# Optimization experiments

Measured on AMD Instinct MI355X. Metric: run time of the kernel, lower is better.

## Reference

```python
import jax, jax.numpy as jnp
import numpy as np

Q, M, KLEN, B = 512, 512, 1024, 4
D, H, DH, G = 1024, 16, 64, 4
DG = D // G          # 256
EPS = 1e-6
SCALE = 1.0 / DH ** 0.5


def _group_ln(x, gamma, beta, n_group):
    # x: [L, B, D]; torch std is unbiased (ddof=1); note (x-mean)/(std+eps)
    L, b, d = x.shape
    xg = x.reshape(L, b, n_group, d // n_group)
    mean = xg.mean(-1, keepdims=True)
    std = jnp.std(xg, axis=-1, ddof=1, keepdims=True)
    out = ((xg - mean) / (std + EPS)).reshape(L, b, d)
    return gamma * out + beta


def _rel_shift(x):
    # x: [q, r, b, n]
    q, r = x.shape[0], x.shape[1]
    zero_pad = jnp.zeros((q, 1) + x.shape[2:], x.dtype)
    x_padded = jnp.concatenate([zero_pad, x], axis=1).reshape((r + 1, q) + x.shape[2:])
    return x_padded[1:].reshape(x.shape)


def setup_inputs() -> dict:
    key = jax.random.key(0)
    ks = jax.random.split(key, 14)
    p = lambda k, s: jax.random.normal(k, s, jnp.float32) * 0.02
    w = jax.random.normal(ks[0], (Q, B, D), jnp.float32)
    r = jax.random.normal(ks[1], (KLEN, 1, D), jnp.float32)
    mems = jax.random.normal(ks[2], (M, B, D), jnp.float32)
    r_w_bias = p(ks[3], (H, DH))
    r_r_bias = p(ks[4], (H, DH))
    gamma_q = jnp.ones((D,), jnp.float32); beta_q = jnp.zeros((D,), jnp.float32)
    gamma_kv = jnp.ones((D,), jnp.float32); beta_kv = jnp.zeros((D,), jnp.float32)
    Wq = p(ks[5], (G, DG, DG))       # grouped conv1d k=1: per-group [out,in]
    Wiq = p(ks[6], (DG, D))          # inter_q_net: conv1d groups=1 [out,in]
    Wk = p(ks[7], (D, D))
    Wv = p(ks[8], (D, D))
    Wr = p(ks[9], (G, DG, DG))       # r_net grouped (n_head*d_head == d_model)
    Wintra = p(ks[10], (G, DG, DG))  # intra_linear grouped conv
    Winter = p(ks[11], (DG, D))      # inter_linear nn.Linear weight
    i = jnp.arange(Q)[:, None]
    j = jnp.arange(KLEN)[None, :]
    attn_mask = (j > i + M)[:, :, None]  # [Q, KLEN, 1] bool, True = masked
    return dict(w=w, r=r, r_w_bias=r_w_bias, r_r_bias=r_r_bias, mems=mems,
                gamma_q=gamma_q, beta_q=beta_q, gamma_kv=gamma_kv, beta_kv=beta_kv,
                Wq=Wq, Wiq=Wiq, Wk=Wk, Wv=Wv, Wr=Wr, Wintra=Wintra, Winter=Winter,
                attn_mask=attn_mask)


def reference(w, r, r_w_bias, r_r_bias, mems, gamma_q, beta_q, gamma_kv, beta_kv,
              Wq, Wiq, Wk, Wv, Wr, Wintra, Winter, attn_mask):
    qlen, bsz, _ = w.shape
    rlen = r.shape[0]
    w_norm = _group_ln(w, gamma_q, beta_q, G)                       # [Q,B,D]
    kv = jnp.concatenate([mems, w], axis=0)
    kv_norm = gamma_kv * (kv - kv.mean(-1, keepdims=True)) / (
        jnp.std(kv, axis=-1, ddof=1, keepdims=True) + EPS) + beta_kv  # [K,B,D]

    # grouped 1x1 conv projections == per-group matmuls
    q_intra = jnp.einsum('qbgd,god->qbgo', w_norm.reshape(qlen, bsz, G, DG), Wq)
    q_global = jnp.einsum('qbd,od->qbo', w_norm, Wiq)               # [Q,B,DG]
    head_q = (q_intra + q_global[:, :, None, :]).reshape(qlen, bsz, H, DH)
    klen = kv_norm.shape[0]
    head_k = jnp.einsum('kbd,od->kbo', kv_norm, Wk).reshape(klen, bsz, H, DH)
    head_v = jnp.einsum('kbd,od->kbo', kv_norm, Wv).reshape(klen, bsz, H, DH)
    r_head_k = jnp.einsum('rgd,god->rgo', r[:, 0].reshape(rlen, G, DG), Wr)
    r_head_k = r_head_k.reshape(rlen, H, DH)                        # [R,H,DH]

    AC = jnp.einsum('ibnd,jbnd->ijbn', head_q + r_w_bias, head_k)
    BD = _rel_shift(jnp.einsum('ibnd,jnd->ijbn', head_q + r_r_bias, r_head_k))
    attn_score = (AC + BD) * SCALE                                  # [Q,K,B,H]
    attn_score = jnp.where(attn_mask[:, :, :, None], -jnp.inf, attn_score)
    attn_prob = jax.nn.softmax(attn_score, axis=1)
    attn_vec = jnp.einsum('ijbn,jbnd->ibnd', attn_prob, head_v)
    attn_out = attn_vec.reshape(qlen, bsz, D)

    inter = jnp.einsum('qbd,od->qbo', attn_out, Winter)             # [Q,B,DG]
    intra = jnp.einsum('qbgd,god->qbgo', attn_out.reshape(qlen, bsz, G, DG), Wintra)
    out = (intra + inter[:, :, None, :]).reshape(qlen, bsz, D)
    return w + out
```

## Files before the change

kernel.cpp:

```cpp
#include <hip/hip_runtime.h>
#include <math.h>

#define Q_LEN 512
#define M_LEN 512
#define KL    1024
#define BSZ   4
#define DM    1024
#define NH    16
#define DHD   64
#define NG    4
#define DGRP  256
#define RL    1024
#define LN_EPS 1e-6f
#define ATT_SCALE 0.125f

typedef short s16x8 __attribute__((ext_vector_type(8)));
typedef float f32x4 __attribute__((ext_vector_type(4)));

__device__ __forceinline__ float wave_sum64(float v) {
#pragma unroll
    for (int off = 32; off > 0; off >>= 1) v += __shfl_xor(v, off);
    return v;
}

__device__ __forceinline__ ushort f2bf(float f) {
    unsigned u = __float_as_uint(f);
    unsigned r = (u + 0x7fffu + ((u >> 16) & 1u)) >> 16;
    return (ushort)r;
}
__device__ __forceinline__ float bf2f(ushort u) {
    return __uint_as_float(((unsigned)u) << 16);
}

__global__ __launch_bounds__(256) void cast8_kernel(
    const float* p0, const float* p1, const float* p2, const float* p3,
    const float* p4, const float* p5, const float* p6, const float* p7,
    ushort* d0, ushort* d1, ushort* d2, ushort* d3,
    ushort* d4, ushort* d5, ushort* d6, ushort* d7)
{
    int bid = blockIdx.x;
    const float* s; ushort* d; int off;
    if      (bid < 1024) { s = p0; d = d0; off = bid; }
    else if (bid < 2048) { s = p1; d = d1; off = bid - 1024; }
    else if (bid < 3072) { s = p2; d = d2; off = bid - 2048; }
    else if (bid < 3328) { s = p3; d = d3; off = bid - 3072; }
    else if (bid < 3584) { s = p4; d = d4; off = bid - 3328; }
    else if (bid < 3840) { s = p5; d = d5; off = bid - 3584; }
    else if (bid < 4096) { s = p6; d = d6; off = bid - 3840; }
    else                 { s = p7; d = d7; off = bid - 4096; }
    int i = off * 1024 + threadIdx.x * 4;
    float4 v = *(const float4*)(s + i);
    ushort4 o;
    o.x = f2bf(v.x); o.y = f2bf(v.y); o.z = f2bf(v.z); o.w = f2bf(v.w);
    *(ushort4*)(d + i) = o;
}

__global__ __launch_bounds__(64) void group_ln_kernel(
    const float* __restrict__ w, const float* __restrict__ gamma,
    const float* __restrict__ beta, ushort* __restrict__ out)
{
    int bid = blockIdx.x;
    int g = bid & (NG - 1);
    long long row = bid >> 2;
    int t = threadIdx.x;
    long long base = row * DM + g * DGRP + t * 4;
    float4 x = *(const float4*)(w + base);
    float mean = wave_sum64(x.x + x.y + x.z + x.w) * (1.0f / 256.0f);
    float dx = x.x - mean, dy = x.y - mean, dz = x.z - mean, dw = x.w - mean;
    float ss = wave_sum64(dx * dx + dy * dy + dz * dz + dw * dw);
    float inv = 1.0f / (sqrtf(ss * (1.0f / 255.0f)) + LN_EPS);
    int db = g * DGRP + t * 4;
    float4 ga = *(const float4*)(gamma + db);
    float4 be = *(const float4*)(beta + db);
    ushort4 o;
    o.x = f2bf(ga.x * (dx * inv) + be.x);
    o.y = f2bf(ga.y * (dy * inv) + be.y);
    o.z = f2bf(ga.z * (dz * inv) + be.z);
    o.w = f2bf(ga.w * (dw * inv) + be.w);
    *(ushort4*)(out + base) = o;
}

__global__ __launch_bounds__(256) void kv_ln_kernel(
    const float* __restrict__ mems, const float* __restrict__ w,
    const float* __restrict__ gamma, const float* __restrict__ beta,
    ushort* __restrict__ out)
{
    int row = blockIdx.x;
    int k = row >> 2, b = row & 3;
    const float* src = (k < M_LEN) ? (mems + ((long long)k * BSZ + b) * DM)
                                   : (w + ((long long)(k - M_LEN) * BSZ + b) * DM);
    int t = threadIdx.x;
    float4 x = *(const float4*)(src + t * 4);
    __shared__ float red[4];
    float s = wave_sum64(x.x + x.y + x.z + x.w);
    int wv = t >> 6, ln = t & 63;
    if (ln == 0) red[wv] = s;
    __syncthreads();
    float mean = (red[0] + red[1] + red[2] + red[3]) * (1.0f / 1024.0f);
    float dx = x.x - mean, dy = x.y - mean, dz = x.z - mean, dw = x.w - mean;
    float ss = wave_sum64(dx * dx + dy * dy + dz * dz + dw * dw);
    __syncthreads();
    if (ln == 0) red[wv] = ss;
    __syncthreads();
    float var = (red[0] + red[1] + red[2] + red[3]) * (1.0f / 1023.0f);
    float inv = 1.0f / (sqrtf(var) + LN_EPS);
    int db = t * 4;
    float4 ga = *(const float4*)(gamma + db);
    float4 be = *(const float4*)(beta + db);
    ushort4 o;
    o.x = f2bf(ga.x * (dx * inv) + be.x);
    o.y = f2bf(ga.y * (dy * inv) + be.y);
    o.z = f2bf(ga.z * (dz * inv) + be.z);
    o.w = f2bf(ga.w * (dw * inv) + be.w);
    *(ushort4*)(out + (long long)row * DM + db) = o;
}

__global__ __launch_bounds__(256) void gemm_bf16_nt(
    const ushort* __restrict__ A, long long aZ, int lda,
    const ushort* __restrict__ W, long long wZ, int ldw,
    float* __restrict__ C, ushort* __restrict__ Cb, long long cZ, int ldc,
    int M, int N, int K,
    const float* __restrict__ add1, long long a1Z, int lda1,
    const float* __restrict__ add2, long long a2Z, int lda2)
{
    int z = blockIdx.z;
    A += (long long)z * aZ;
    W += (long long)z * wZ;
    if (C)  C += (long long)z * cZ;
    if (Cb) Cb += (long long)z * cZ;
    if (add1) add1 += (long long)z * a1Z;
    if (add2) add2 += (long long)z * a2Z;
    int m0 = blockIdx.y * 64, n0 = blockIdx.x * 64;
    int t = threadIdx.x;
    int lane = t & 63, wid = t >> 6;
    int wr = wid >> 1, wc = wid & 1;
    int srow = t >> 2, scol = (t & 3) * 16;
    int fr = lane & 15, kq = (lane >> 4) * 8;

    __shared__ __align__(16) ushort As[64][72];
    __shared__ __align__(16) ushort Ws[64][72];

    f32x4 acc00 = {}, acc01 = {}, acc10 = {}, acc11 = {};

    const ushort* Arow = A + (long long)(m0 + srow) * lda + scol;
    const ushort* Wrow = W + (long long)(n0 + srow) * ldw + scol;

    s16x8 ra0 = *(const s16x8*)Arow;
    s16x8 ra1 = *(const s16x8*)(Arow + 8);
    s16x8 rw0 = *(const s16x8*)Wrow;
    s16x8 rw1 = *(const s16x8*)(Wrow + 8);
    *(s16x8*)&As[srow][scol] = ra0; *(s16x8*)&As[srow][scol + 8] = ra1;
    *(s16x8*)&Ws[srow][scol] = rw0; *(s16x8*)&Ws[srow][scol + 8] = rw1;
    __syncthreads();

    for (int k0 = 0; k0 < K; k0 += 64) {
        bool hasNext = (k0 + 64) < K;
        if (hasNext) {
            ra0 = *(const s16x8*)(Arow + k0 + 64);
            ra1 = *(const s16x8*)(Arow + k0 + 72);
            rw0 = *(const s16x8*)(Wrow + k0 + 64);
            rw1 = *(const s16x8*)(Wrow + k0 + 72);
        }
#pragma unroll
        for (int kk = 0; kk < 64; kk += 32) {
            s16x8 a0 = *(const s16x8*)&As[wr * 32 + fr][kk + kq];
            s16x8 a1 = *(const s16x8*)&As[wr * 32 + 16 + fr][kk + kq];
            s16x8 b0 = *(const s16x8*)&Ws[wc * 32 + fr][kk + kq];
            s16x8 b1 = *(const s16x8*)&Ws[wc * 32 + 16 + fr][kk + kq];
            acc00 = __builtin_amdgcn_mfma_f32_16x16x32_bf16(a0, b0, acc00, 0, 0, 0);
            acc01 = __builtin_amdgcn_mfma_f32_16x16x32_bf16(a0, b1, acc01, 0, 0, 0);
            acc10 = __builtin_amdgcn_mfma_f32_16x16x32_bf16(a1, b0, acc10, 0, 0, 0);
            acc11 = __builtin_amdgcn_mfma_f32_16x16x32_bf16(a1, b1, acc11, 0, 0, 0);
        }
        __syncthreads();
        if (hasNext) {
            *(s16x8*)&As[srow][scol] = ra0; *(s16x8*)&As[srow][scol + 8] = ra1;
            *(s16x8*)&Ws[srow][scol] = rw0; *(s16x8*)&Ws[srow][scol + 8] = rw1;
            __syncthreads();
        }
    }

    int rbase = (lane >> 4) * 4;
#pragma unroll
    for (int p = 0; p < 4; ++p) {
        int mrow0 = wr * 32 + rbase + p;
        int mrow1 = mrow0 + 16;
        int ncol0 = wc * 32 + fr;
        int ncol1 = ncol0 + 16;
        float v00 = acc00[p], v01 = acc01[p], v10 = acc10[p], v11 = acc11[p];
        long long r0 = m0 + mrow0, r1 = m0 + mrow1;
        int c0 = n0 + ncol0, c1 = n0 + ncol1;
        if (add1) {
            v00 += add1[r0 * lda1 + c0]; v01 += add1[r0 * lda1 + c1];
            v10 += add1[r1 * lda1 + c0]; v11 += add1[r1 * lda1 + c1];
        }
        if (add2) {
            v00 += add2[r0 * lda2 + c0]; v01 += add2[r0 * lda2 + c1];
            v10 += add2[r1 * lda2 + c0]; v11 += add2[r1 * lda2 + c1];
        }
        if (Cb) {
            Cb[r0 * ldc + c0] = f2bf(v00); Cb[r0 * ldc + c1] = f2bf(v01);
            Cb[r1 * ldc + c0] = f2bf(v10); Cb[r1 * ldc + c1] = f2bf(v11);
        } else {
            C[r0 * ldc + c0] = v00; C[r0 * ldc + c1] = v01;
            C[r1 * ldc + c0] = v10; C[r1 * ldc + c1] = v11;
        }
    }
}

__global__ __launch_bounds__(256) void transpose_v_kernel(
    const ushort* __restrict__ vin, ushort* __restrict__ vout)
{
    __shared__ __align__(16) ushort T[64][72];
    int bn = blockIdx.y;
    int b = bn >> 4, n = bn & 15;
    int k0 = blockIdx.x * 64;
    int t = threadIdx.x;
    {
        int kr = t >> 2, dp = (t & 3) * 16;
        const ushort* sp = vin + (((long long)(k0 + kr)) * 4 + b) * DM + n * DHD + dp;
        *(s16x8*)&T[kr][dp] = *(const s16x8*)sp;
        *(s16x8*)&T[kr][dp + 8] = *(const s16x8*)(sp + 8);
    }
    __syncthreads();
    {
        int d = t >> 2, kp = (t & 3) * 16;
        ushort vals[16];
#pragma unroll
        for (int q = 0; q < 16; ++q) vals[q] = T[kp + q][d];
        ushort* dp = vout + ((long long)bn * DHD + d) * KL + k0 + kp;
        *(s16x8*)dp = *(const s16x8*)&vals[0];
        *(s16x8*)(dp + 8) = *(const s16x8*)&vals[8];
    }
}

__global__ __launch_bounds__(256) void corr_kernel(
    const ushort* __restrict__ r_hk, const float* __restrict__ rwb,
    const float* __restrict__ rrb, float* __restrict__ corr)
{
    int n = blockIdx.y;
    int k = blockIdx.x * 4 + (threadIdx.x >> 6);
    int d = threadIdx.x & 63;
    float diff = rrb[n * DHD + d] - rwb[n * DHD + d];
    float v = diff * bf2f(r_hk[(long long)k * DM + n * DHD + d]);
    v = wave_sum64(v);
    if (d == 0) corr[n * RL + k] = v;
}

__global__ __launch_bounds__(256) void attn_mfma_kernel(
    const ushort* __restrict__ hq, const ushort* __restrict__ hk,
    const ushort* __restrict__ hvT, const ushort* __restrict__ rhk,
    const float* __restrict__ corr, ushort* __restrict__ attn_out)
{
    __shared__ __align__(16) ushort Ks[2][64][72];
    __shared__ __align__(16) ushort VsT[2][64][72];
    __shared__ __align__(16) ushort RKs[128][72];
    __shared__ __align__(16) ushort BDs[64][128];
    __shared__ __align__(16) ushort Ps[64][64];

    int bh = blockIdx.y;
    int b = bh >> 4, n = bh & 15;
    int i0 = blockIdx.x * 64;
    int t = threadIdx.x;
    int lane = t & 63, w = t >> 6;
    int lr16 = lane & 15;
    int lk8 = (lane >> 4) * 8;
    int orow = (lane >> 4) * 4;
    int swzBD = ((lane >> 4) & 3) << 4;

    s16x8 qf0, qf1;
    {
        const ushort* qp = hq + (((long long)(i0 + w * 16 + lr16)) * 4 + b) * DM
                              + n * DHD + lk8;
        qf0 = *(const s16x8*)qp;
        qf1 = *(const s16x8*)(qp + 32);
    }

    f32x4 O[4] = {};
    float m_[4], l_[4];
#pragma unroll
    for (int r = 0; r < 4; ++r) { m_[r] = -INFINITY; l_[r] = 0.0f; }

    int nJ = ((i0 + 575) >> 6) + 1;
    if (nJ > 16) nJ = 16;
    int ka0 = 448 - i0;

    int srow = t >> 2, sdp = (t & 3) * 16;

    {
        const ushort* kp = hk + (((long long)srow) * 4 + b) * DM + n * DHD + sdp;
        *(s16x8*)&Ks[0][srow][sdp] = *(const s16x8*)kp;
        *(s16x8*)&Ks[0][srow][sdp + 8] = *(const s16x8*)(kp + 8);
        const ushort* vp = hvT + ((long long)bh * DHD + srow) * KL + sdp;
        *(s16x8*)&VsT[0][srow][sdp] = *(const s16x8*)vp;
        *(s16x8*)&VsT[0][srow][sdp + 8] = *(const s16x8*)(vp + 8);
        int rr = t >> 1, dp2 = (t & 1) * 32;
        int rabs = ka0 + rr;
        const ushort* rp = rhk + (long long)rabs * DM + n * DHD + dp2;
        int phys = rabs & 127;
#pragma unroll
        for (int q = 0; q < 4; ++q)
            *(s16x8*)&RKs[phys][dp2 + q * 8] = *(const s16x8*)(rp + q * 8);
    }
    __syncthreads();

    int cur = 0;
    for (int jt = 0; jt < nJ; ++jt) {
        int j0 = jt * 64;
        int ka = ka0 + j0;
        bool hasNext = (jt + 1) < nJ;

        s16x8 pk0 = {}, pk1 = {}, pv0 = {}, pv1 = {}, pr0 = {}, pr1 = {};
        if (hasNext) {
            int j0n = j0 + 64;
            const ushort* kp = hk + (((long long)(j0n + srow)) * 4 + b) * DM + n * DHD + sdp;
            pk0 = *(const s16x8*)kp;
            pk1 = *(const s16x8*)(kp + 8);
            const ushort* vp = hvT + ((long long)bh * DHD + srow) * KL + j0n + sdp;
            pv0 = *(const s16x8*)vp;
            pv1 = *(const s16x8*)(vp + 8);
            int rnew = ka + 128 + srow;
            if (rnew < RL) {
                const ushort* rp = rhk + (long long)rnew * DM + n * DHD + sdp;
                pr0 = *(const s16x8*)rp;
                pr1 = *(const s16x8*)(rp + 8);
            }
        }

        f32x4 ac[4] = {};
#pragma unroll
        for (int nb = 0; nb < 4; ++nb) {
            s16x8 kb0 = *(const s16x8*)&Ks[cur][nb * 16 + lr16][lk8];
            s16x8 kb1 = *(const s16x8*)&Ks[cur][nb * 16 + lr16][32 + lk8];
            ac[nb] = __builtin_amdgcn_mfma_f32_16x16x32_bf16(qf0, kb0, ac[nb], 0, 0, 0);
            ac[nb] = __builtin_amdgcn_mfma_f32_16x16x32_bf16(qf1, kb1, ac[nb], 0, 0, 0);
        }
        int nb0 = (jt == 0) ? 0 : 4;
        for (int nb = nb0; nb < 8; ++nb) {
            int kk = nb * 16 + lr16;
            int rabs = ka + kk;
            int phys = rabs & 127;
            f32x4 bd = {};
            s16x8 rb0 = *(const s16x8*)&RKs[phys][lk8];
            s16x8 rb1 = *(const s16x8*)&RKs[phys][32 + lk8];
            bd = __builtin_amdgcn_mfma_f32_16x16x32_bf16(qf0, rb0, bd, 0, 0, 0);
            bd = __builtin_amdgcn_mfma_f32_16x16x32_bf16(qf1, rb1, bd, 0, 0, 0);
            float cadd = (rabs < RL) ? corr[n * RL + rabs] : 0.0f;
            int colw = phys ^ swzBD;
#pragma unroll
            for (int reg = 0; reg < 4; ++reg)
                BDs[w * 16 + orow + reg][colw] = f2bf(bd[reg] + cadd);
        }
        if (jt == 0) __syncthreads();

        float pvv[4][4], rowm[4];
#pragma unroll
        for (int reg = 0; reg < 4; ++reg) {
            int il = w * 16 + orow + reg;
            int i = i0 + il;
            rowm[reg] = -INFINITY;
#pragma unroll
            for (int nb = 0; nb < 4; ++nb) {
                int jc = nb * 16 + lr16;
                int j = j0 + jc;
                float s = -INFINITY;
                if (j <= i + M_LEN) {
                    int phys = (j + 511 - i) & 127;
                    s = (ac[nb][reg] + bf2f(BDs[il][phys ^ swzBD])) * ATT_SCALE;
                }
                pvv[reg][nb] = s;
                rowm[reg] = fmaxf(rowm[reg], s);
            }
        }
#pragma unroll
        for (int st = 1; st <= 8; st <<= 1)
#pragma unroll
            for (int reg = 0; reg < 4; ++reg)
                rowm[reg] = fmaxf(rowm[reg], __shfl_xor(rowm[reg], st));
        float rs[4], alpha[4];
#pragma unroll
        for (int reg = 0; reg < 4; ++reg) {
            int il = w * 16 + orow + reg;
            float newm = fmaxf(m_[reg], rowm[reg]);
            alpha[reg] = __expf(m_[reg] - newm);
            m_[reg] = newm;
            rs[reg] = 0.0f;
#pragma unroll
            for (int nb = 0; nb < 4; ++nb) {
                float p = __expf(pvv[reg][nb] - newm);
                rs[reg] += p;
                int jc = nb * 16 + lr16;
                int colp = (((jc >> 3) ^ (il & 7)) << 3) | (jc & 7);
                Ps[il][colp] = f2bf(p);
            }
        }
#pragma unroll
        for (int st = 1; st <= 8; st <<= 1)
#pragma unroll
            for (int reg = 0; reg < 4; ++reg)
                rs[reg] += __shfl_xor(rs[reg], st);
#pragma unroll
        for (int reg = 0; reg < 4; ++reg) {
            l_[reg] = l_[reg] * alpha[reg] + rs[reg];
#pragma unroll
            for (int nb = 0; nb < 4; ++nb) O[nb][reg] *= alpha[reg];
        }

        {
            int prow = w * 16 + lr16;
            int rh = prow & 7;
#pragma unroll
            for (int kc = 0; kc < 2; ++kc) {
                int blk = kc * 4 + (lane >> 4);
                s16x8 pa = *(const s16x8*)&Ps[prow][(blk ^ rh) << 3];
#pragma unroll
                for (int nb = 0; nb < 4; ++nb) {
                    s16x8 vb = *(const s16x8*)&VsT[cur][nb * 16 + lr16][kc * 32 + lk8];
                    O[nb] = __builtin_amdgcn_mfma_f32_16x16x32_bf16(pa, vb, O[nb], 0, 0, 0);
                }
            }
        }

        if (hasNext) {
            *(s16x8*)&Ks[cur ^ 1][srow][sdp] = pk0;
            *(s16x8*)&Ks[cur ^ 1][srow][sdp + 8] = pk1;
            *(s16x8*)&VsT[cur ^ 1][srow][sdp] = pv0;
            *(s16x8*)&VsT[cur ^ 1][srow][sdp + 8] = pv1;
            int phys = (ka + 128 + srow) & 127;
            *(s16x8*)&RKs[phys][sdp] = pr0;
            *(s16x8*)&RKs[phys][sdp + 8] = pr1;
        }
        __syncthreads();
        cur ^= 1;
    }

#pragma unroll
    for (int reg = 0; reg < 4; ++reg) {
        int il = w * 16 + orow + reg;
        long long i = i0 + il;
        float inv = 1.0f / l_[reg];
#pragma unroll
        for (int nb = 0; nb < 4; ++nb)
            attn_out[(i * 4 + b) * DM + n * DHD + nb * 16 + lr16] = f2bf(O[nb][reg] * inv);
    }
}

extern "C" void kernel_launch(void* const* d_in, const int* in_sizes, int n_in,
                              void* d_out, int out_size, void* d_ws, size_t ws_size,
                              hipStream_t stream) {
    const float* w       = (const float*)d_in[0];
    const float* r       = (const float*)d_in[1];
    const float* rwb     = (const float*)d_in[2];
    const float* rrb     = (const float*)d_in[3];
    const float* mems    = (const float*)d_in[4];
    const float* gamma_q = (const float*)d_in[5];
    const float* beta_q  = (const float*)d_in[6];
    const float* gamma_kv= (const float*)d_in[7];
    const float* beta_kv = (const float*)d_in[8];
    const float* Wq      = (const float*)d_in[9];
    const float* Wiq     = (const float*)d_in[10];
    const float* Wk      = (const float*)d_in[11];
    const float* Wv      = (const float*)d_in[12];
    const float* Wr      = (const float*)d_in[13];
    const float* Wintra  = (const float*)d_in[14];
    const float* Winter  = (const float*)d_in[15];
    float* out = (float*)d_out;
    float* ws = (float*)d_ws;

    float* tmp  = ws;
    float* corr = tmp + 524288;

    ushort* w_norm_bf  = (ushort*)(corr + 16384);
    ushort* kv_norm_bf = w_norm_bf + 2097152;
    ushort* head_q_bf  = kv_norm_bf + 4194304;
    ushort* head_k_bf  = head_q_bf + 2097152;
    ushort* head_v_bf  = head_k_bf + 4194304;
    ushort* head_vT_bf = head_v_bf + 4194304;
    ushort* r_hk_bf    = head_vT_bf + 4194304;
    ushort* attn_o_bf  = r_hk_bf + 1048576;
    ushort* r_bf       = attn_o_bf + 2097152;
    ushort* Wk_bf      = r_bf + 1048576;
    ushort* Wv_bf      = Wk_bf + 1048576;
    ushort* Wq_bf      = Wv_bf + 1048576;
    ushort* Wiq_bf     = Wq_bf + 262144;
    ushort* Wr_bf      = Wiq_bf + 262144;
    ushort* Wintra_bf  = Wr_bf + 262144;
    ushort* Winter_bf  = Wintra_bf + 262144;

    group_ln_kernel<<<dim3(Q_LEN * BSZ * NG), 64, 0, stream>>>(w, gamma_q, beta_q, w_norm_bf);
    kv_ln_kernel<<<dim3(KL * BSZ), 256, 0, stream>>>(mems, w, gamma_kv, beta_kv, kv_norm_bf);

    cast8_kernel<<<dim3(4352), 256, 0, stream>>>(
        r, Wk, Wv, Wq, Wiq, Wr, Wintra, Winter,
        r_bf, Wk_bf, Wv_bf, Wq_bf, Wiq_bf, Wr_bf, Wintra_bf, Winter_bf);

    gemm_bf16_nt<<<dim3(16, 64, 2), 256, 0, stream>>>(
        kv_norm_bf, 0, DM, Wk_bf, 1048576, DM, nullptr, head_k_bf, 4194304, DM,
        KL * BSZ, DM, DM, nullptr, 0, 0, nullptr, 0, 0);
    transpose_v_kernel<<<dim3(16, 64), 256, 0, stream>>>(head_v_bf, head_vT_bf);

    gemm_bf16_nt<<<dim3(4, 32, 1), 256, 0, stream>>>(
        w_norm_bf, 0, DM, Wiq_bf, 0, DM, tmp, nullptr, 0, DGRP, Q_LEN * BSZ, DGRP, DM,
        nullptr, 0, 0, nullptr, 0, 0);
    gemm_bf16_nt<<<dim3(4, 32, 4), 256, 0, stream>>>(
        w_norm_bf, DGRP, DM, Wq_bf, DGRP * DGRP, DGRP, nullptr, head_q_bf, DGRP, DM,
        Q_LEN * BSZ, DGRP, DGRP, tmp, 0, DGRP, rwb, DGRP, 0);
    gemm_bf16_nt<<<dim3(4, 16, 4), 256, 0, stream>>>(
        r_bf, DGRP, DM, Wr_bf, DGRP * DGRP, DGRP, nullptr, r_hk_bf, DGRP, DM,
        RL, DGRP, DGRP, nullptr, 0, 0, nullptr, 0, 0);

    corr_kernel<<<dim3(RL / 4, NH), 256, 0, stream>>>(r_hk_bf, rwb, rrb, corr);

    attn_mfma_kernel<<<dim3(Q_LEN / 64, BSZ * NH), 256, 0, stream>>>(
        head_q_bf, head_k_bf, head_vT_bf, r_hk_bf, corr, attn_o_bf);

    gemm_bf16_nt<<<dim3(4, 32, 1), 256, 0, stream>>>(
        attn_o_bf, 0, DM, Winter_bf, 0, DM, tmp, nullptr, 0, DGRP, Q_LEN * BSZ, DGRP, DM,
        nullptr, 0, 0, nullptr, 0, 0);
    gemm_bf16_nt<<<dim3(4, 32, 4), 256, 0, stream>>>(
        attn_o_bf, DGRP, DM, Wintra_bf, DGRP * DGRP, DGRP, out, nullptr, DGRP, DM,
        Q_LEN * BSZ, DGRP, DGRP, tmp, 0, DGRP, w, DGRP, DM);
}
```

Baseline: 174.8 us.

## Fold grouped and global projections into augmented weights; add 128-tile K/V GEMM

The grouped intra projection and the shared inter projection are merged into one dense augmented weight per output group, built on device by adding the block-diagonal group weights into the broadcast inter weight. The q-side and output-side projections then each need a single GEMM with K=1024 instead of two GEMMs plus a fp32 temp buffer round trip. The K/V projection moves to a new 128x128-tile MFMA GEMM to get more reuse per block. The trade-off is a per-call weight-augmentation kernel and four times the FLOPs on the grouped part, since it becomes dense.

```diff
diff --git a/kernel.cpp b/kernel.cpp
--- a/kernel.cpp
+++ b/kernel.cpp
@@ -32,27 +32,43 @@
     return __uint_as_float(((unsigned)u) << 16);
 }
 
-__global__ __launch_bounds__(256) void cast8_kernel(
+__global__ __launch_bounds__(256) void cast4_kernel(
     const float* p0, const float* p1, const float* p2, const float* p3,
-    const float* p4, const float* p5, const float* p6, const float* p7,
-    ushort* d0, ushort* d1, ushort* d2, ushort* d3,
-    ushort* d4, ushort* d5, ushort* d6, ushort* d7)
+    ushort* d0, ushort* d1, ushort* d2, ushort* d3)
 {
     int bid = blockIdx.x;
     const float* s; ushort* d; int off;
     if      (bid < 1024) { s = p0; d = d0; off = bid; }
     else if (bid < 2048) { s = p1; d = d1; off = bid - 1024; }
     else if (bid < 3072) { s = p2; d = d2; off = bid - 2048; }
-    else if (bid < 3328) { s = p3; d = d3; off = bid - 3072; }
-    else if (bid < 3584) { s = p4; d = d4; off = bid - 3328; }
-    else if (bid < 3840) { s = p5; d = d5; off = bid - 3584; }
-    else if (bid < 4096) { s = p6; d = d6; off = bid - 3840; }
-    else                 { s = p7; d = d7; off = bid - 4096; }
+    else                 { s = p3; d = d3; off = bid - 3072; }
     int i = off * 1024 + threadIdx.x * 4;
     float4 v = *(const float4*)(s + i);
     ushort4 o;
     o.x = f2bf(v.x); o.y = f2bf(v.y); o.z = f2bf(v.z); o.w = f2bf(v.w);
     *(ushort4*)(d + i) = o;
+}
+
+__global__ __launch_bounds__(256) void augment_kernel(
+    const float* __restrict__ Wg0, const float* __restrict__ Wf0, ushort* __restrict__ Wo0,
+    const float* __restrict__ Wg1, const float* __restrict__ Wf1, ushort* __restrict__ Wo1)
+{
+    int bid = blockIdx.x;
+    const float* Wg; const float* Wf; ushort* Wo; int off;
+    if (bid < 1024) { Wg = Wg0; Wf = Wf0; Wo = Wo0; off = bid; }
+    else            { Wg = Wg1; Wf = Wf1; Wo = Wo1; off = bid - 1024; }
+    int idx = off * 1024 + threadIdx.x * 4;
+    int g = idx >> 18;
+    int o = (idx >> 10) & 255;
+    int k = idx & 1023;
+    float4 v = *(const float4*)(Wf + o * 1024 + k);
+    if ((k >> 8) == g) {
+        float4 vg = *(const float4*)(Wg + ((g * 256 + o) << 8) + (k & 255));
+        v.x += vg.x; v.y += vg.y; v.z += vg.z; v.w += vg.w;
+    }
+    ushort4 u;
+    u.x = f2bf(v.x); u.y = f2bf(v.y); u.z = f2bf(v.z); u.w = f2bf(v.w);
+    *(ushort4*)(Wo + idx) = u;
 }
 
 __global__ __launch_bounds__(64) void group_ln_kernel(
@@ -113,6 +129,74 @@
     o.z = f2bf(ga.z * (dz * inv) + be.z);
     o.w = f2bf(ga.w * (dw * inv) + be.w);
     *(ushort4*)(out + (long long)row * DM + db) = o;
+}
+
+__global__ __launch_bounds__(256) void gemm128_bf16_nt(
+    const ushort* __restrict__ A, int lda,
+    const ushort* __restrict__ W, long long wZ, int ldw,
+    ushort* __restrict__ Cb, long long cZ, int ldc, int K)
+{
+    int z = blockIdx.z;
+    W += (long long)z * wZ;
+    Cb += (long long)z * cZ;
+    int m0 = blockIdx.y * 128, n0 = blockIdx.x * 128;
+    int t = threadIdx.x, lane = t & 63, w = t >> 6;
+    int wr = w >> 1, wc = w & 1;
+    int fr = lane & 15, kq = (lane >> 4) * 8;
+    int srow = t >> 1, scol = (t & 1) * 16;
+
+    __shared__ __align__(16) ushort As[128][40];
+    __shared__ __align__(16) ushort Ws[128][40];
+
+    const ushort* Ar = A + (long long)(m0 + srow) * lda + scol;
+    const ushort* Wr = W + (long long)(n0 + srow) * ldw + scol;
+
+    f32x4 acc[16] = {};
+
+    s16x8 a0 = *(const s16x8*)Ar, a1 = *(const s16x8*)(Ar + 8);
+    s16x8 b0 = *(const s16x8*)Wr, b1 = *(const s16x8*)(Wr + 8);
+    *(s16x8*)&As[srow][scol] = a0; *(s16x8*)&As[srow][scol + 8] = a1;
+    *(s16x8*)&Ws[srow][scol] = b0; *(s16x8*)&Ws[srow][scol + 8] = b1;
+    __syncthreads();
+
+    for (int k0 = 0; k0 < K; k0 += 32) {
+        bool more = (k0 + 32) < K;
+        if (more) {
+            a0 = *(const s16x8*)(Ar + k0 + 32); a1 = *(const s16x8*)(Ar + k0 + 40);
+            b0 = *(const s16x8*)(Wr + k0 + 32); b1 = *(const s16x8*)(Wr + k0 + 40);
+        }
+        s16x8 af[4], bf_[4];
+#pragma unroll
+        for (int rb = 0; rb < 4; ++rb)
+            af[rb] = *(const s16x8*)&As[wr * 64 + rb * 16 + fr][kq];
+#pragma unroll
+        for (int cb = 0; cb < 4; ++cb)
+            bf_[cb] = *(const s16x8*)&Ws[wc * 64 + cb * 16 + fr][kq];
+#pragma unroll
+        for (int rb = 0; rb < 4; ++rb)
+#pragma unroll
+            for (int cb = 0; cb < 4; ++cb)
+                acc[rb * 4 + cb] = __builtin_amdgcn_mfma_f32_16x16x32_bf16(
+                    af[rb], bf_[cb], acc[rb * 4 + cb], 0, 0, 0);
+        __syncthreads();
+        if (more) {
+            *(s16x8*)&As[srow][scol] = a0; *(s16x8*)&As[srow][scol + 8] = a1;
+            *(s16x8*)&Ws[srow][scol] = b0; *(s16x8*)&Ws[srow][scol + 8] = b1;
+            __syncthreads();
+        }
+    }
+
+    int rbase = (lane >> 4) * 4;
+#pragma unroll
+    for (int rb = 0; rb < 4; ++rb)
+#pragma unroll
+        for (int p = 0; p < 4; ++p) {
+            long long row = m0 + wr * 64 + rb * 16 + rbase + p;
+            ushort* crow = Cb + row * ldc + n0 + wc * 64 + fr;
+#pragma unroll
+            for (int cb = 0; cb < 4; ++cb)
+                crow[cb * 16] = f2bf(acc[rb * 4 + cb][p]);
+        }
 }
 
 __global__ __launch_bounds__(256) void gemm_bf16_nt(
@@ -467,8 +551,7 @@
     float* out = (float*)d_out;
     float* ws = (float*)d_ws;
 
-    float* tmp  = ws;
-    float* corr = tmp + 524288;
+    float* corr = ws;
 
     ushort* w_norm_bf  = (ushort*)(corr + 16384);
     ushort* kv_norm_bf = w_norm_bf + 2097152;
@@ -481,30 +564,25 @@
     ushort* r_bf       = attn_o_bf + 2097152;
     ushort* Wk_bf      = r_bf + 1048576;
     ushort* Wv_bf      = Wk_bf + 1048576;
-    ushort* Wq_bf      = Wv_bf + 1048576;
-    ushort* Wiq_bf     = Wq_bf + 262144;
-    ushort* Wr_bf      = Wiq_bf + 262144;
-    ushort* Wintra_bf  = Wr_bf + 262144;
-    ushort* Winter_bf  = Wintra_bf + 262144;
+    ushort* Wr_bf      = Wv_bf + 1048576;
+    ushort* Wq_aug     = Wr_bf + 262144;
+    ushort* Wo_aug     = Wq_aug + 1048576;
 
     group_ln_kernel<<<dim3(Q_LEN * BSZ * NG), 64, 0, stream>>>(w, gamma_q, beta_q, w_norm_bf);
     kv_ln_kernel<<<dim3(KL * BSZ), 256, 0, stream>>>(mems, w, gamma_kv, beta_kv, kv_norm_bf);
 
-    cast8_kernel<<<dim3(4352), 256, 0, stream>>>(
-        r, Wk, Wv, Wq, Wiq, Wr, Wintra, Winter,
-        r_bf, Wk_bf, Wv_bf, Wq_bf, Wiq_bf, Wr_bf, Wintra_bf, Winter_bf);
-
-    gemm_bf16_nt<<<dim3(16, 64, 2), 256, 0, stream>>>(
-        kv_norm_bf, 0, DM, Wk_bf, 1048576, DM, nullptr, head_k_bf, 4194304, DM,
-        KL * BSZ, DM, DM, nullptr, 0, 0, nullptr, 0, 0);
+    cast4_kernel<<<dim3(3328), 256, 0, stream>>>(
+        r, Wk, Wv, Wr, r_bf, Wk_bf, Wv_bf, Wr_bf);
+    augment_kernel<<<dim3(2048), 256, 0, stream>>>(
+        Wq, Wiq, Wq_aug, Wintra, Winter, Wo_aug);
+
+    gemm128_bf16_nt<<<dim3(8, 32, 2), 256, 0, stream>>>(
+        kv_norm_bf, DM, Wk_bf, 1048576, DM, head_k_bf, 4194304, DM, DM);
     transpose_v_kernel<<<dim3(16, 64), 256, 0, stream>>>(head_v_bf, head_vT_bf);
 
-    gemm_bf16_nt<<<dim3(4, 32, 1), 256, 0, stream>>>(
-        w_norm_bf, 0, DM, Wiq_bf, 0, DM, tmp, nullptr, 0, DGRP, Q_LEN * BSZ, DGRP, DM,
-        nullptr, 0, 0, nullptr, 0, 0);
     gemm_bf16_nt<<<dim3(4, 32, 4), 256, 0, stream>>>(
-        w_norm_bf, DGRP, DM, Wq_bf, DGRP * DGRP, DGRP, nullptr, head_q_bf, DGRP, DM,
-        Q_LEN * BSZ, DGRP, DGRP, tmp, 0, DGRP, rwb, DGRP, 0);
+        w_norm_bf, 0, DM, Wq_aug, 262144, DM, nullptr, head_q_bf, DGRP, DM,
+        Q_LEN * BSZ, DGRP, DM, nullptr, 0, 0, rwb, DGRP, 0);
     gemm_bf16_nt<<<dim3(4, 16, 4), 256, 0, stream>>>(
         r_bf, DGRP, DM, Wr_bf, DGRP * DGRP, DGRP, nullptr, r_hk_bf, DGRP, DM,
         RL, DGRP, DGRP, nullptr, 0, 0, nullptr, 0, 0);
@@ -514,10 +592,7 @@
     attn_mfma_kernel<<<dim3(Q_LEN / 64, BSZ * NH), 256, 0, stream>>>(
         head_q_bf, head_k_bf, head_vT_bf, r_hk_bf, corr, attn_o_bf);
 
-    gemm_bf16_nt<<<dim3(4, 32, 1), 256, 0, stream>>>(
-        attn_o_bf, 0, DM, Winter_bf, 0, DM, tmp, nullptr, 0, DGRP, Q_LEN * BSZ, DGRP, DM,
-        nullptr, 0, 0, nullptr, 0, 0);
     gemm_bf16_nt<<<dim3(4, 32, 4), 256, 0, stream>>>(
-        attn_o_bf, DGRP, DM, Wintra_bf, DGRP * DGRP, DGRP, out, nullptr, DGRP, DM,
-        Q_LEN * BSZ, DGRP, DGRP, tmp, 0, DGRP, w, DGRP, DM);
-}
+        attn_o_bf, 0, DM, Wo_aug, 262144, DM, out, nullptr, DGRP, DM,
+        Q_LEN * BSZ, DGRP, DM, w, DGRP, DM, nullptr, 0, 0);
+}
```

New measurement: 163.6 us. -6.4%, faster.
